# Kernel tuning notes

Measured on AMD Instinct MI355X. Metric: run time of the kernel, lower is better.

The kernel has to match this reference:

```python
import jax, jax.numpy as jnp
import numpy as np

B, C, N, K = 16, 128, 1024, 16
QK_DIM, V_DIM = 64, 128


def setup_inputs() -> dict:
    key = jax.random.key(0)
    k1, k2, k3, k4, k5 = jax.random.split(key, 5)
    return {
        "input_tensor": jax.random.normal(k1, (B, C, N, K), dtype=jnp.float32),
        "W_qk": jax.random.normal(k2, (2 * QK_DIM, C), dtype=jnp.float32) * 0.05,
        "b_qk": jax.random.normal(k3, (2 * QK_DIM,), dtype=jnp.float32) * 0.01,
        "W_v": jax.random.normal(k4, (V_DIM, C), dtype=jnp.float32) * 0.05,
        "b_v": jax.random.normal(k5, (V_DIM,), dtype=jnp.float32) * 0.01,
        "qk_dim": QK_DIM,
    }


def reference(input_tensor, W_qk, b_qk, W_v, b_v, qk_dim):
    # 1x1 conv == channel matmul: [B,C,N,K] x [2*qk,C] -> [B,2*qk,N,K]
    combine = jnp.einsum('bcnk,oc->bonk', input_tensor, W_qk) + b_qk[None, :, None, None]
    q = combine[:, :qk_dim]          # [B, qk, N, K]
    k = combine[:, qk_dim:]          # [B, qk, N, K]
    # per-point attention over neighbor axis
    energy = jnp.einsum('bcnq,bcnk->bnqk', q, k)            # [B, N, K, K]
    scale = jnp.asarray(qk_dim, energy.dtype) ** 0.5
    attention = jax.nn.softmax(energy / scale, axis=3)       # softmax over last k
    v = jnp.einsum('bcnk,oc->bonk', input_tensor, W_v) + b_v[None, :, None, None]  # [B, v, N, K]
    attention_first = attention[:, :, :, 0]                  # [B, N, K] (q-axis slice at k=0)
    # out = einsum('bnk,bcnk->bnkc') then sum over k -> fuse into one einsum
    output = jnp.einsum('bnk,bcnk->bnc', attention_first, v) # [B, N, v_dim]
    return output
```

## Files before the change

kernel.cpp:

```cpp
#include <hip/hip_runtime.h>
#include <hip/hip_bf16.h>
#include <stdint.h>

typedef __attribute__((ext_vector_type(4))) float f32x4;
typedef __attribute__((ext_vector_type(8))) short s16x8;

__device__ __forceinline__ unsigned int pack_bf2(float lo, float hi) {
  union { __hip_bfloat162 h; unsigned int u; } cv;
  cv.h = __float22bfloat162_rn(float2{lo, hi});
  return cv.u;
}
__device__ __forceinline__ float bflo(unsigned int w) { return __uint_as_float(w << 16); }
__device__ __forceinline__ float bfhi(unsigned int w) { return __uint_as_float(w & 0xFFFF0000u); }

union FragU { uint4 u; s16x8 s; };

__global__ void __launch_bounds__(256) prep_weights(const float* __restrict__ Wqk,
                                                    const float* __restrict__ Wv,
                                                    uint16_t* __restrict__ wsqk,
                                                    uint16_t* __restrict__ wsv) {
  int i = blockIdx.x * 256 + threadIdx.x;
  if (i < 16384) {
    union { __hip_bfloat16 h; uint16_t u; } c; c.h = __float2bfloat16(Wqk[i]);
    wsqk[i] = c.u;
  } else if (i < 32768) {
    int j = i - 16384;
    union { __hip_bfloat16 h; uint16_t u; } c; c.h = __float2bfloat16(Wv[j]);
    wsv[j] = c.u;
  }
}

__global__ void __launch_bounds__(256, 4) attn_kernel(
    const float* __restrict__ X,
    const float* __restrict__ bqk,
    const float* __restrict__ bv,
    const unsigned int* __restrict__ wqk,
    const unsigned int* __restrict__ wv,
    float* __restrict__ out)
{
  __shared__ unsigned int sXt[64 * 68];
  __shared__ unsigned int sP[64 * 68];
  __shared__ float sa[4][16];
  __shared__ float sS[4];

  const int t    = threadIdx.x;
  const int lane = t & 63;
  const int w    = t >> 6;
  const int nn   = lane & 15;
  const int quad = lane >> 4;

  const int b  = blockIdx.x >> 8;
  const int n0 = (blockIdx.x & 255) << 2;
  const int n  = n0 + w;

  FragU xf[4];
  {
    const float* __restrict__ xb = X + (size_t)b * (128 * 1024 * 16) + n * 16 + nn;
    #pragma unroll
    for (int ks = 0; ks < 4; ++ks) {
      const int c0 = ks * 32 + quad * 8;
      float v[8];
      #pragma unroll
      for (int i = 0; i < 8; ++i)
        v[i] = xb[(size_t)(c0 + i) * (1024 * 16)];
      xf[ks].u.x = pack_bf2(v[0], v[1]);
      xf[ks].u.y = pack_bf2(v[2], v[3]);
      xf[ks].u.z = pack_bf2(v[4], v[5]);
      xf[ks].u.w = pack_bf2(v[6], v[7]);
      *reinterpret_cast<uint4*>(&sXt[(w * 16 + nn) * 68 + ks * 16 + quad * 4]) = xf[ks].u;
    }
  }

  f32x4 acc[8];
  {
    #pragma unroll
    for (int mt = 0; mt < 8; ++mt) {
      const float4 bq = *reinterpret_cast<const float4*>(bqk + mt * 16 + quad * 4);
      acc[mt][0] = bq.x; acc[mt][1] = bq.y; acc[mt][2] = bq.z; acc[mt][3] = bq.w;
    }
    #pragma unroll
    for (int ks = 0; ks < 4; ++ks) {
      #pragma unroll
      for (int mt = 0; mt < 8; ++mt) {
        FragU af;
        af.u = *reinterpret_cast<const uint4*>(wqk + (mt * 16 + nn) * 64 + ks * 16 + quad * 4);
        acc[mt] = __builtin_amdgcn_mfma_f32_16x16x32_bf16(af.s, xf[ks].s, acc[mt], 0, 0, 0);
      }
    }
  }

  {
    #pragma unroll
    for (int mt = 0; mt < 8; ++mt) {
      uint2 pr;
      pr.x = pack_bf2(acc[mt][0], acc[mt][1]);
      pr.y = pack_bf2(acc[mt][2], acc[mt][3]);
      *reinterpret_cast<uint2*>(&sP[(w * 16 + nn) * 68 + mt * 8 + quad * 2]) = pr;
    }
  }

  float aq[16];
  float Ssum;
  {
    f32x4 e = {0.f, 0.f, 0.f, 0.f};
    #pragma unroll
    for (int ks = 0; ks < 2; ++ks) {
      FragU qa, kb;
      qa.u = *reinterpret_cast<const uint4*>(&sP[(w * 16 + nn) * 68 + ks * 16 + quad * 4]);
      kb.u = *reinterpret_cast<const uint4*>(&sP[(w * 16 + nn) * 68 + 32 + ks * 16 + quad * 4]);
      e = __builtin_amdgcn_mfma_f32_16x16x32_bf16(qa.s, kb.s, e, 0, 0, 0);
    }
    #pragma unroll
    for (int r = 0; r < 4; ++r) {
      float l = e[r] * 0.125f;
      float mx = l;
      mx = fmaxf(mx, __shfl_xor(mx, 1));
      mx = fmaxf(mx, __shfl_xor(mx, 2));
      mx = fmaxf(mx, __shfl_xor(mx, 4));
      mx = fmaxf(mx, __shfl_xor(mx, 8));
      float pe = __expf(l - mx);
      float ss = pe;
      ss += __shfl_xor(ss, 1);
      ss += __shfl_xor(ss, 2);
      ss += __shfl_xor(ss, 4);
      ss += __shfl_xor(ss, 8);
      if (nn == 0) sa[w][quad * 4 + r] = pe / ss;
    }
    Ssum = 0.f;
    #pragma unroll
    for (int k = 0; k < 16; ++k) { aq[k] = sa[w][k]; Ssum += aq[k]; }
  }

  unsigned int* sYw = &sP[w * 16 * 68];
  {
    float y0 = 0.f, y1 = 0.f;
    #pragma unroll
    for (int k = 0; k < 16; ++k) {
      const unsigned int xw = sXt[(w * 16 + k) * 68 + lane];
      y0 += aq[k] * bflo(xw);
      y1 += aq[k] * bfhi(xw);
    }
    sYw[lane] = pack_bf2(y0, y1);
    if (lane == 0) sS[w] = Ssum;
  }
  __syncthreads();

  {
    #pragma unroll
    for (int i = 0; i < 2; ++i) {
      const int ct = w * 2 + i;
      f32x4 z = {0.f, 0.f, 0.f, 0.f};
      #pragma unroll
      for (int ks = 0; ks < 4; ++ks) {
        FragU av2, by;
        av2.u = *reinterpret_cast<const uint4*>(wv + (ct * 16 + nn) * 64 + ks * 16 + quad * 4);
        by.u  = *reinterpret_cast<const uint4*>(&sP[(nn & 3) * 16 * 68 + ks * 16 + quad * 4]);
        z = __builtin_amdgcn_mfma_f32_16x16x32_bf16(av2.s, by.s, z, 0, 0, 0);
      }
      if (nn < 4) {
        const float4 bvv = *reinterpret_cast<const float4*>(bv + ct * 16 + quad * 4);
        const float S = sS[nn];
        float4 o4;
        o4.x = z[0] + bvv.x * S;
        o4.y = z[1] + bvv.y * S;
        o4.z = z[2] + bvv.z * S;
        o4.w = z[3] + bvv.w * S;
        *reinterpret_cast<float4*>(out + (size_t)(b * 1024 + n0 + nn) * 128 + ct * 16 + quad * 4) = o4;
      }
    }
  }
}

extern "C" void kernel_launch(void* const* d_in, const int* in_sizes, int n_in,
                              void* d_out, int out_size, void* d_ws, size_t ws_size,
                              hipStream_t stream) {
  (void)in_sizes; (void)n_in; (void)out_size; (void)ws_size;
  const float* X   = (const float*)d_in[0];
  const float* Wqk = (const float*)d_in[1];
  const float* bqk = (const float*)d_in[2];
  const float* Wv  = (const float*)d_in[3];
  const float* bv  = (const float*)d_in[4];

  uint16_t* wsqk = (uint16_t*)d_ws;
  uint16_t* wsv  = wsqk + 16384;

  prep_weights<<<128, 256, 0, stream>>>(Wqk, Wv, wsqk, wsv);
  attn_kernel<<<4096, 256, 0, stream>>>(X, bqk, bv,
                                        (const unsigned int*)wsqk,
                                        (const unsigned int*)wsv,
                                        (float*)d_out);
}
```

Before: 253.6 us.

## Split QK projection across waves by output tile, sharing X tiles through LDS

Each wave used to compute all 8 QK output tiles for its own point and load the whole QK weight matrix from global memory. Now each wave computes 2 output-channel tiles for all 4 points in the block, reading X fragments for every point from shared memory. This cuts per-wave weight traffic and register pressure from the full weight matrix. In exchange it adds two block-wide barriers and more LDS reads.

```diff
diff --git a/kernel.cpp b/kernel.cpp
--- a/kernel.cpp
+++ b/kernel.cpp
@@ -51,11 +51,9 @@
 
   const int b  = blockIdx.x >> 8;
   const int n0 = (blockIdx.x & 255) << 2;
-  const int n  = n0 + w;
-
-  FragU xf[4];
-  {
-    const float* __restrict__ xb = X + (size_t)b * (128 * 1024 * 16) + n * 16 + nn;
+
+  {
+    const float* __restrict__ xb = X + (size_t)b * (128 * 1024 * 16) + (n0 + w) * 16 + nn;
     #pragma unroll
     for (int ks = 0; ks < 4; ++ks) {
       const int c0 = ks * 32 + quad * 8;
@@ -63,41 +61,60 @@
       #pragma unroll
       for (int i = 0; i < 8; ++i)
         v[i] = xb[(size_t)(c0 + i) * (1024 * 16)];
-      xf[ks].u.x = pack_bf2(v[0], v[1]);
-      xf[ks].u.y = pack_bf2(v[2], v[3]);
-      xf[ks].u.z = pack_bf2(v[4], v[5]);
-      xf[ks].u.w = pack_bf2(v[6], v[7]);
-      *reinterpret_cast<uint4*>(&sXt[(w * 16 + nn) * 68 + ks * 16 + quad * 4]) = xf[ks].u;
-    }
-  }
-
-  f32x4 acc[8];
-  {
-    #pragma unroll
-    for (int mt = 0; mt < 8; ++mt) {
-      const float4 bq = *reinterpret_cast<const float4*>(bqk + mt * 16 + quad * 4);
-      acc[mt][0] = bq.x; acc[mt][1] = bq.y; acc[mt][2] = bq.z; acc[mt][3] = bq.w;
+      uint4 xw;
+      xw.x = pack_bf2(v[0], v[1]);
+      xw.y = pack_bf2(v[2], v[3]);
+      xw.z = pack_bf2(v[4], v[5]);
+      xw.w = pack_bf2(v[6], v[7]);
+      *reinterpret_cast<uint4*>(&sXt[(w * 16 + nn) * 68 + ks * 16 + quad * 4]) = xw;
+    }
+  }
+  __syncthreads();
+
+  f32x4 acc[2][4];
+  {
+    FragU af[2][4];
+    #pragma unroll
+    for (int i = 0; i < 2; ++i)
+      #pragma unroll
+      for (int ks = 0; ks < 4; ++ks)
+        af[i][ks].u = *reinterpret_cast<const uint4*>(
+            wqk + ((2 * w + i) * 16 + nn) * 64 + ks * 16 + quad * 4);
+    #pragma unroll
+    for (int i = 0; i < 2; ++i) {
+      const float4 bq = *reinterpret_cast<const float4*>(bqk + (2 * w + i) * 16 + quad * 4);
+      #pragma unroll
+      for (int n = 0; n < 4; ++n) {
+        acc[i][n][0] = bq.x; acc[i][n][1] = bq.y;
+        acc[i][n][2] = bq.z; acc[i][n][3] = bq.w;
+      }
     }
     #pragma unroll
     for (int ks = 0; ks < 4; ++ks) {
-      #pragma unroll
-      for (int mt = 0; mt < 8; ++mt) {
-        FragU af;
-        af.u = *reinterpret_cast<const uint4*>(wqk + (mt * 16 + nn) * 64 + ks * 16 + quad * 4);
-        acc[mt] = __builtin_amdgcn_mfma_f32_16x16x32_bf16(af.s, xf[ks].s, acc[mt], 0, 0, 0);
-      }
-    }
-  }
-
-  {
-    #pragma unroll
-    for (int mt = 0; mt < 8; ++mt) {
-      uint2 pr;
-      pr.x = pack_bf2(acc[mt][0], acc[mt][1]);
-      pr.y = pack_bf2(acc[mt][2], acc[mt][3]);
-      *reinterpret_cast<uint2*>(&sP[(w * 16 + nn) * 68 + mt * 8 + quad * 2]) = pr;
-    }
-  }
+      FragU bf[4];
+      #pragma unroll
+      for (int n = 0; n < 4; ++n)
+        bf[n].u = *reinterpret_cast<const uint4*>(&sXt[(n * 16 + nn) * 68 + ks * 16 + quad * 4]);
+      #pragma unroll
+      for (int i = 0; i < 2; ++i)
+        #pragma unroll
+        for (int n = 0; n < 4; ++n)
+          acc[i][n] = __builtin_amdgcn_mfma_f32_16x16x32_bf16(af[i][ks].s, bf[n].s, acc[i][n], 0, 0, 0);
+    }
+  }
+
+  {
+    #pragma unroll
+    for (int i = 0; i < 2; ++i)
+      #pragma unroll
+      for (int n = 0; n < 4; ++n) {
+        uint2 pr;
+        pr.x = pack_bf2(acc[i][n][0], acc[i][n][1]);
+        pr.y = pack_bf2(acc[i][n][2], acc[i][n][3]);
+        *reinterpret_cast<uint2*>(&sP[(n * 16 + nn) * 68 + (2 * w + i) * 8 + quad * 2]) = pr;
+      }
+  }
+  __syncthreads();
 
   float aq[16];
   float Ssum;
```

Result: faster. 222.8 us (-12.2%).
